# Kernel tuning notes

Measured on AMD Instinct MI355X. Metric: run time of the kernel, lower is better.

Reference implementation:

```python
import jax, jax.numpy as jnp
import numpy as np

NEG_INF = -9e15  # matches torch's -9000000000000000.0 mask value
ALPHA = 0.2      # leakyrelu slope for attention scores
OUT_SLOPE = 0.01 # default F.leaky_relu slope on the output


def setup_inputs() -> dict:
    key = jax.random.key(0)
    k = jax.random.split(key, 6)
    B, Ns, Nt = 4, 4096, 4096
    Fs, Ft, Fo = 256, 256, 64
    h = jax.random.normal(k[0], (B, Nt, Ft), dtype=jnp.float32)
    ctx = jax.random.normal(k[1], (B, Ns, Fs), dtype=jnp.float32)
    adj = jax.random.randint(k[2], (B, Nt, Ns), 0, 2, dtype=jnp.int32)
    Ws = jax.random.normal(k[3], (Fs, Fo), dtype=jnp.float32) * (1.414 * (6.0 / (Fs + Fo)) ** 0.5)
    Wt = jax.random.normal(k[4], (Ft, Fo), dtype=jnp.float32) * (1.414 * (6.0 / (Ft + Fo)) ** 0.5)
    a = jax.random.normal(k[5], (2 * Fo, 1), dtype=jnp.float32) * (1.414 * (6.0 / (2 * Fo + 1)) ** 0.5)
    return {"h": h, "ctx": ctx, "adj": adj, "Ws": Ws, "Wt": Wt, "a": a}


def _leaky(x, slope):
    return jnp.where(x > 0, x, slope * x)


def reference(h, ctx, adj, Ws, Wt, a):
    Fo = Ws.shape[1]
    Ws_ctx = jnp.einsum('bsf,fo->bso', ctx, Ws)   # [B, Ns, Fo]
    Wt_h = jnp.einsum('btf,fo->bto', h, Wt)       # [B, Nt, Fo]
    B, Ns, _ = Ws_ctx.shape
    Nt = Wt_h.shape[1]
    # a_input @ a decomposes: score(i,j) = Ws_ctx[i]@a[:Fo] + Wt_h[j]@a[Fo:]
    s = Ws_ctx @ a[:Fo, 0]  # [B, Ns]
    t = Wt_h @ a[Fo:, 0]    # [B, Nt]
    # Original builds flat order i*Nt + j (i over Ns, j over Nt), then views as [B, Nt, Ns].
    raw = s[:, :, None] + t[:, None, :]           # [B, Ns, Nt], flat index i*Nt+j
    e = _leaky(raw, ALPHA).reshape(B, Nt, Ns)     # faithful reshape
    masked = jnp.where(adj > 0, e, jnp.full_like(e, NEG_INF))
    attn = jax.nn.softmax(masked, axis=2)         # [B, Nt, Ns]
    h_prime = jnp.einsum('bts,bso->bto', attn, Ws_ctx)
    return _leaky(h_prime, OUT_SLOPE)
```

## Files before the change

### kernel.cpp

```cpp
#include <hip/hip_runtime.h>

#define BB 4
#define NS 4096
#define NT 4096
#define FS 256
#define FT 256
#define FO 64
#define ALPHA 0.2f
#define OUT_SLOPE 0.01f
#define L2E 1.4426950408889634f

typedef __attribute__((ext_vector_type(8))) short short8;
typedef __attribute__((ext_vector_type(4))) float floatx4;

__device__ __forceinline__ float leaky(float x, float s) { return x > 0.f ? x : s * x; }
__device__ __forceinline__ float leaky_max(float x, float s) { return fmaxf(x, s * x); }

__device__ __forceinline__ short f2bf(float x) {
  union { float f; unsigned u; } c; c.f = x;
  unsigned r = c.u + 0x7fffu + ((c.u >> 16) & 1u);
  return (short)(r >> 16);
}

__device__ __forceinline__ unsigned cvt_pk_bf16(float lo, float hi) {
  unsigned r;
  asm("v_cvt_pk_bf16_f32 %0, %1, %2" : "=v"(r) : "v"(lo), "v"(hi));
  return r;
}

__global__ void k_wa(const float* __restrict__ Wt, const float* __restrict__ a,
                     float* __restrict__ wa) {
  int f = threadIdx.x;
  float acc = 0.f;
#pragma unroll
  for (int o = 0; o < FO; ++o) acc += Wt[f * FO + o] * a[FO + o];
  wa[f] = acc * L2E;
}

__global__ __launch_bounds__(256) void k_t(const float* __restrict__ h,
                                           const float* __restrict__ wa,
                                           float* __restrict__ tvec) {
  int lane = threadIdx.x & 63, wave = threadIdx.x >> 6;
  int row = blockIdx.x * 4 + wave;
  const float4* hp = (const float4*)(h + (size_t)row * FT);
  const float4* wp = (const float4*)wa;
  float4 hv = hp[lane], wv = wp[lane];
  float acc = hv.x * wv.x + hv.y * wv.y + hv.z * wv.z + hv.w * wv.w;
#pragma unroll
  for (int off = 32; off; off >>= 1) acc += __shfl_down(acc, off);
  if (lane == 0) tvec[row] = acc;
}

__global__ __launch_bounds__(256) void k_tmax(const float* __restrict__ tvec,
                                              float* __restrict__ tmax) {
  __shared__ float red[256];
  int b = blockIdx.x, tid = threadIdx.x;
  float m = -3.0e38f;
  for (int j = tid; j < NS; j += 256) m = fmaxf(m, tvec[b * NS + j]);
  red[tid] = m;
  __syncthreads();
  for (int s = 128; s; s >>= 1) {
    if (tid < s) red[tid] = fmaxf(red[tid], red[tid + s]);
    __syncthreads();
  }
  if (tid == 0) tmax[b] = red[0];
}

__global__ __launch_bounds__(256) void k_wsctx(const float* __restrict__ ctx,
                                               const float* __restrict__ Ws,
                                               const float* __restrict__ a,
                                               short* __restrict__ vT,
                                               float* __restrict__ svec) {
  const int f = threadIdx.x & 63, wave = threadIdx.x >> 6;
  const int row0 = blockIdx.x * 16 + wave * 4;
  const float4* c0 = (const float4*)(ctx + (size_t)(row0 + 0) * FS);
  const float4* c1 = (const float4*)(ctx + (size_t)(row0 + 1) * FS);
  const float4* c2 = (const float4*)(ctx + (size_t)(row0 + 2) * FS);
  const float4* c3 = (const float4*)(ctx + (size_t)(row0 + 3) * FS);
  float r0 = 0.f, r1 = 0.f, r2 = 0.f, r3 = 0.f;
#pragma unroll 2
  for (int k4 = 0; k4 < FS / 4; ++k4) {
    const float w0 = Ws[(k4 * 4 + 0) * FO + f];
    const float w1 = Ws[(k4 * 4 + 1) * FO + f];
    const float w2 = Ws[(k4 * 4 + 2) * FO + f];
    const float w3 = Ws[(k4 * 4 + 3) * FO + f];
    float4 x;
    x = c0[k4]; r0 += x.x * w0 + x.y * w1 + x.z * w2 + x.w * w3;
    x = c1[k4]; r1 += x.x * w0 + x.y * w1 + x.z * w2 + x.w * w3;
    x = c2[k4]; r2 += x.x * w0 + x.y * w1 + x.z * w2 + x.w * w3;
    x = c3[k4]; r3 += x.x * w0 + x.y * w1 + x.z * w2 + x.w * w3;
  }
  const int b = row0 >> 12;
  const int rloc = row0 & (NS - 1);
  short* vp = vT + ((size_t)b * FO + f) * NS + rloc;
  vp[0] = f2bf(r0); vp[1] = f2bf(r1); vp[2] = f2bf(r2); vp[3] = f2bf(r3);

  const float af = a[f] * L2E;
  float s0 = r0 * af, s1 = r1 * af, s2 = r2 * af, s3 = r3 * af;
#pragma unroll
  for (int off = 32; off; off >>= 1) {
    s0 += __shfl_down(s0, off);
    s1 += __shfl_down(s1, off);
    s2 += __shfl_down(s2, off);
    s3 += __shfl_down(s3, off);
  }
  if (f == 0) {
    svec[row0 + 0] = s0;
    svec[row0 + 1] = s1;
    svec[row0 + 2] = s2;
    svec[row0 + 3] = s3;
  }
}

template <int JS>
__global__ __launch_bounds__(256) void k_part(const int* __restrict__ adj,
                                              const short* __restrict__ vT,
                                              const float* __restrict__ svec,
                                              const float* __restrict__ tvec,
                                              const float* __restrict__ tmax,
                                              float* __restrict__ outpart,
                                              float* __restrict__ lpart) {
  const int lane = threadIdx.x & 63;
  const int wv = threadIdx.x >> 6;
  const int m = lane & 15;
  const int q = lane >> 4;

  constexpr int LOG = (JS == 8) ? 3 : 2;
  const int tile = blockIdx.x >> LOG;
  const int js = blockIdx.x & (JS - 1);
  const int b = tile >> 6;
  const int i0 = (tile & 63) * 64;
  const int jbase = js * (NS / JS);

  const int r = i0 + wv * 16 + m;
  const float sr = svec[b * NS + r];
  const float cr = leaky_max(sr + tmax[b], ALPHA);

  const int* arow = adj + ((size_t)(b * NT) + r) * NS + jbase;
  const float* tp = tvec + b * NS + jbase;
  const short* vp0 = vT + ((size_t)b * FO + m) * NS + jbase;

  floatx4 acc0 = {0.f, 0.f, 0.f, 0.f};
  floatx4 acc1 = {0.f, 0.f, 0.f, 0.f};
  floatx4 acc2 = {0.f, 0.f, 0.f, 0.f};
  floatx4 acc3 = {0.f, 0.f, 0.f, 0.f};
  float lsum = 0.f;

#pragma unroll 2
  for (int jc = 0; jc < (NS / JS) / 32; ++jc) {
    const int j0 = jc * 32 + q * 8;
    const int4 a0 = *(const int4*)(arow + j0);
    const int4 a1 = *(const int4*)(arow + j0 + 4);
    const float4 t0 = *(const float4*)(tp + j0);
    const float4 t1 = *(const float4*)(tp + j0 + 4);

    float w[8];
    w[0] = (a0.x > 0) ? __builtin_amdgcn_exp2f(leaky_max(sr + t0.x, ALPHA) - cr) : 0.f;
    w[1] = (a0.y > 0) ? __builtin_amdgcn_exp2f(leaky_max(sr + t0.y, ALPHA) - cr) : 0.f;
    w[2] = (a0.z > 0) ? __builtin_amdgcn_exp2f(leaky_max(sr + t0.z, ALPHA) - cr) : 0.f;
    w[3] = (a0.w > 0) ? __builtin_amdgcn_exp2f(leaky_max(sr + t0.w, ALPHA) - cr) : 0.f;
    w[4] = (a1.x > 0) ? __builtin_amdgcn_exp2f(leaky_max(sr + t1.x, ALPHA) - cr) : 0.f;
    w[5] = (a1.y > 0) ? __builtin_amdgcn_exp2f(leaky_max(sr + t1.y, ALPHA) - cr) : 0.f;
    w[6] = (a1.z > 0) ? __builtin_amdgcn_exp2f(leaky_max(sr + t1.z, ALPHA) - cr) : 0.f;
    w[7] = (a1.w > 0) ? __builtin_amdgcn_exp2f(leaky_max(sr + t1.w, ALPHA) - cr) : 0.f;

    lsum += ((w[0] + w[1]) + (w[2] + w[3])) + ((w[4] + w[5]) + (w[6] + w[7]));

    union { short8 s; unsigned u[4]; } afu;
    afu.u[0] = cvt_pk_bf16(w[0], w[1]);
    afu.u[1] = cvt_pk_bf16(w[2], w[3]);
    afu.u[2] = cvt_pk_bf16(w[4], w[5]);
    afu.u[3] = cvt_pk_bf16(w[6], w[7]);
    const short8 af = afu.s;

    const short8 bf0 = *(const short8*)(vp0 + 0 * 16 * NS + j0);
    const short8 bf1 = *(const short8*)(vp0 + 1 * 16 * NS + j0);
    const short8 bf2 = *(const short8*)(vp0 + 2 * 16 * NS + j0);
    const short8 bf3 = *(const short8*)(vp0 + 3 * 16 * NS + j0);
    acc0 = __builtin_amdgcn_mfma_f32_16x16x32_bf16(af, bf0, acc0, 0, 0, 0);
    acc1 = __builtin_amdgcn_mfma_f32_16x16x32_bf16(af, bf1, acc1, 0, 0, 0);
    acc2 = __builtin_amdgcn_mfma_f32_16x16x32_bf16(af, bf2, acc2, 0, 0, 0);
    acc3 = __builtin_amdgcn_mfma_f32_16x16x32_bf16(af, bf3, acc3, 0, 0, 0);
  }

  float v = lsum;
  v += __shfl_down(v, 32);
  v += __shfl_down(v, 16);
  if (lane < 16) lpart[(size_t)js * BB * NT + (size_t)b * NT + i0 + wv * 16 + m] = v;

  float* op = outpart + (size_t)js * BB * NT * FO +
              ((size_t)(b * NT) + i0 + wv * 16 + q * 4) * FO + m;
#pragma unroll
  for (int reg = 0; reg < 4; ++reg) {
    op[(size_t)reg * FO + 0 * 16] = acc0[reg];
    op[(size_t)reg * FO + 1 * 16] = acc1[reg];
    op[(size_t)reg * FO + 2 * 16] = acc2[reg];
    op[(size_t)reg * FO + 3 * 16] = acc3[reg];
  }
}

template <int JS>
__global__ __launch_bounds__(256) void k_fin(const float* __restrict__ outpart,
                                             const float* __restrict__ lpart,
                                             float* __restrict__ out) {
  const size_t NP = (size_t)BB * NT * FO;
  const int idx = blockIdx.x * 256 + threadIdx.x;
  const int row = idx >> 4;
  float l = 0.f;
#pragma unroll
  for (int s = 0; s < JS; ++s) l += lpart[(size_t)s * BB * NT + row];
  const float inv = 1.f / l;
  float4 acc = {0.f, 0.f, 0.f, 0.f};
#pragma unroll
  for (int s = 0; s < JS; ++s) {
    float4 v = ((const float4*)(outpart + (size_t)s * NP))[idx];
    acc.x += v.x; acc.y += v.y; acc.z += v.z; acc.w += v.w;
  }
  float4 o;
  o.x = leaky_max(acc.x * inv, OUT_SLOPE);
  o.y = leaky_max(acc.y * inv, OUT_SLOPE);
  o.z = leaky_max(acc.z * inv, OUT_SLOPE);
  o.w = leaky_max(acc.w * inv, OUT_SLOPE);
  ((float4*)out)[idx] = o;
}

extern "C" void kernel_launch(void* const* d_in, const int* in_sizes, int n_in,
                              void* d_out, int out_size, void* d_ws, size_t ws_size,
                              hipStream_t stream) {
  const float* h   = (const float*)d_in[0];
  const float* ctx = (const float*)d_in[1];
  const int*   adj = (const int*)d_in[2];
  const float* Ws  = (const float*)d_in[3];
  const float* Wt  = (const float*)d_in[4];
  const float* a   = (const float*)d_in[5];
  float* out = (float*)d_out;
  float* ws = (float*)d_ws;

  const size_t np = (size_t)BB * NT * FO;
  const size_t fixed_f = 2 * (size_t)BB * NS + 256 + 4;
  const size_t vt_bytes = (size_t)BB * FO * NS * 2;
  const size_t need8 = ((size_t)8 * np + (size_t)8 * BB * NT + fixed_f) * sizeof(float) + vt_bytes;
  const int js = (ws_size >= need8) ? 8 : 4;

  float* outpart = ws;
  float* lpart   = outpart + (size_t)js * np;
  float* tvec    = lpart + (size_t)js * BB * NT;
  float* svec    = tvec + BB * NS;
  float* wa      = svec + BB * NS;
  float* tmax    = wa + 256;
  short* vT      = (short*)(tmax + 4);

  k_wa<<<1, 256, 0, stream>>>(Wt, a, wa);
  k_t<<<(BB * NT) / 4, 256, 0, stream>>>(h, wa, tvec);
  k_tmax<<<BB, 256, 0, stream>>>(tvec, tmax);
  k_wsctx<<<(BB * NS) / 16, 256, 0, stream>>>(ctx, Ws, a, vT, svec);
  if (js == 8) {
    k_part<8><<<(BB * NT / 64) * 8, 256, 0, stream>>>(adj, vT, svec, tvec, tmax,
                                                      outpart, lpart);
    k_fin<8><<<(BB * NT * FO / 4) / 256, 256, 0, stream>>>(outpart, lpart, out);
  } else {
    k_part<4><<<(BB * NT / 64) * 4, 256, 0, stream>>>(adj, vT, svec, tvec, tmax,
                                                      outpart, lpart);
    k_fin<4><<<(BB * NT * FO / 4) / 256, 256, 0, stream>>>(outpart, lpart, out);
  }
}
```

Measured before the change: 511.2 us.

## Software-pipeline k_part loads with double-buffered registers and fix split at 4

Restructures the main loop of the attention partial kernel into a two-stage register double buffer. The adj, t and V loads for the next chunk are issued before the exp/MFMA work on the current chunk, with scheduling barriers holding that order. It also adds a launch-bounds occupancy hint and hardcodes a j-split of 4 instead of picking 8 when workspace allows. The aim is to hide the latency of global loads from the streamed adjacency; the costs are higher register pressure and, if 8 was being chosen before, fewer blocks in flight.

```diff
diff --git a/kernel.cpp b/kernel.cpp
--- a/kernel.cpp
+++ b/kernel.cpp
@@ -8,12 +8,12 @@
 #define FO 64
 #define ALPHA 0.2f
 #define OUT_SLOPE 0.01f
+#define JSPLIT 4
 #define L2E 1.4426950408889634f
 
 typedef __attribute__((ext_vector_type(8))) short short8;
 typedef __attribute__((ext_vector_type(4))) float floatx4;
 
-__device__ __forceinline__ float leaky(float x, float s) { return x > 0.f ? x : s * x; }
 __device__ __forceinline__ float leaky_max(float x, float s) { return fmaxf(x, s * x); }
 
 __device__ __forceinline__ short f2bf(float x) {
@@ -113,19 +113,20 @@
 }
 
 template <int JS>
-__global__ __launch_bounds__(256) void k_part(const int* __restrict__ adj,
-                                              const short* __restrict__ vT,
-                                              const float* __restrict__ svec,
-                                              const float* __restrict__ tvec,
-                                              const float* __restrict__ tmax,
-                                              float* __restrict__ outpart,
-                                              float* __restrict__ lpart) {
+__global__ __launch_bounds__(256, 4) void k_part(const int* __restrict__ adj,
+                                                 const short* __restrict__ vT,
+                                                 const float* __restrict__ svec,
+                                                 const float* __restrict__ tvec,
+                                                 const float* __restrict__ tmax,
+                                                 float* __restrict__ outpart,
+                                                 float* __restrict__ lpart) {
   const int lane = threadIdx.x & 63;
   const int wv = threadIdx.x >> 6;
   const int m = lane & 15;
   const int q = lane >> 4;
 
   constexpr int LOG = (JS == 8) ? 3 : 2;
+  constexpr int NC = (NS / JS) / 32;
   const int tile = blockIdx.x >> LOG;
   const int js = blockIdx.x & (JS - 1);
   const int b = tile >> 6;
@@ -146,42 +147,60 @@
   floatx4 acc3 = {0.f, 0.f, 0.f, 0.f};
   float lsum = 0.f;
 
-#pragma unroll 2
-  for (int jc = 0; jc < (NS / JS) / 32; ++jc) {
-    const int j0 = jc * 32 + q * 8;
-    const int4 a0 = *(const int4*)(arow + j0);
-    const int4 a1 = *(const int4*)(arow + j0 + 4);
-    const float4 t0 = *(const float4*)(tp + j0);
-    const float4 t1 = *(const float4*)(tp + j0 + 4);
-
-    float w[8];
-    w[0] = (a0.x > 0) ? __builtin_amdgcn_exp2f(leaky_max(sr + t0.x, ALPHA) - cr) : 0.f;
-    w[1] = (a0.y > 0) ? __builtin_amdgcn_exp2f(leaky_max(sr + t0.y, ALPHA) - cr) : 0.f;
-    w[2] = (a0.z > 0) ? __builtin_amdgcn_exp2f(leaky_max(sr + t0.z, ALPHA) - cr) : 0.f;
-    w[3] = (a0.w > 0) ? __builtin_amdgcn_exp2f(leaky_max(sr + t0.w, ALPHA) - cr) : 0.f;
-    w[4] = (a1.x > 0) ? __builtin_amdgcn_exp2f(leaky_max(sr + t1.x, ALPHA) - cr) : 0.f;
-    w[5] = (a1.y > 0) ? __builtin_amdgcn_exp2f(leaky_max(sr + t1.y, ALPHA) - cr) : 0.f;
-    w[6] = (a1.z > 0) ? __builtin_amdgcn_exp2f(leaky_max(sr + t1.z, ALPHA) - cr) : 0.f;
-    w[7] = (a1.w > 0) ? __builtin_amdgcn_exp2f(leaky_max(sr + t1.w, ALPHA) - cr) : 0.f;
-
-    lsum += ((w[0] + w[1]) + (w[2] + w[3])) + ((w[4] + w[5]) + (w[6] + w[7]));
-
-    union { short8 s; unsigned u[4]; } afu;
-    afu.u[0] = cvt_pk_bf16(w[0], w[1]);
-    afu.u[1] = cvt_pk_bf16(w[2], w[3]);
-    afu.u[2] = cvt_pk_bf16(w[4], w[5]);
-    afu.u[3] = cvt_pk_bf16(w[6], w[7]);
-    const short8 af = afu.s;
-
-    const short8 bf0 = *(const short8*)(vp0 + 0 * 16 * NS + j0);
-    const short8 bf1 = *(const short8*)(vp0 + 1 * 16 * NS + j0);
-    const short8 bf2 = *(const short8*)(vp0 + 2 * 16 * NS + j0);
-    const short8 bf3 = *(const short8*)(vp0 + 3 * 16 * NS + j0);
-    acc0 = __builtin_amdgcn_mfma_f32_16x16x32_bf16(af, bf0, acc0, 0, 0, 0);
-    acc1 = __builtin_amdgcn_mfma_f32_16x16x32_bf16(af, bf1, acc1, 0, 0, 0);
-    acc2 = __builtin_amdgcn_mfma_f32_16x16x32_bf16(af, bf2, acc2, 0, 0, 0);
-    acc3 = __builtin_amdgcn_mfma_f32_16x16x32_bf16(af, bf3, acc3, 0, 0, 0);
-  }
+  int4 Aa0, Aa1; float4 At0, At1; short8 Av0, Av1, Av2, Av3;
+  int4 Ba0, Ba1; float4 Bt0, Bt1; short8 Bv0, Bv1, Bv2, Bv3;
+
+#define ISSUE(S, jc) do {                                        \
+    const int j0_ = (jc) * 32 + q * 8;                           \
+    S##a0 = *(const int4*)(arow + j0_);                          \
+    S##a1 = *(const int4*)(arow + j0_ + 4);                      \
+    S##t0 = *(const float4*)(tp + j0_);                          \
+    S##t1 = *(const float4*)(tp + j0_ + 4);                      \
+    S##v0 = *(const short8*)(vp0 + 0 * 16 * NS + j0_);           \
+    S##v1 = *(const short8*)(vp0 + 1 * 16 * NS + j0_);           \
+    S##v2 = *(const short8*)(vp0 + 2 * 16 * NS + j0_);           \
+    S##v3 = *(const short8*)(vp0 + 3 * 16 * NS + j0_);           \
+  } while (0)
+
+#define COMPUTE(S) do {                                                         \
+    float w0 = (S##a0.x > 0) ? __builtin_amdgcn_exp2f(leaky_max(sr + S##t0.x, ALPHA) - cr) : 0.f; \
+    float w1 = (S##a0.y > 0) ? __builtin_amdgcn_exp2f(leaky_max(sr + S##t0.y, ALPHA) - cr) : 0.f; \
+    float w2 = (S##a0.z > 0) ? __builtin_amdgcn_exp2f(leaky_max(sr + S##t0.z, ALPHA) - cr) : 0.f; \
+    float w3 = (S##a0.w > 0) ? __builtin_amdgcn_exp2f(leaky_max(sr + S##t0.w, ALPHA) - cr) : 0.f; \
+    float w4 = (S##a1.x > 0) ? __builtin_amdgcn_exp2f(leaky_max(sr + S##t1.x, ALPHA) - cr) : 0.f; \
+    float w5 = (S##a1.y > 0) ? __builtin_amdgcn_exp2f(leaky_max(sr + S##t1.y, ALPHA) - cr) : 0.f; \
+    float w6 = (S##a1.z > 0) ? __builtin_amdgcn_exp2f(leaky_max(sr + S##t1.z, ALPHA) - cr) : 0.f; \
+    float w7 = (S##a1.w > 0) ? __builtin_amdgcn_exp2f(leaky_max(sr + S##t1.w, ALPHA) - cr) : 0.f; \
+    lsum += ((w0 + w1) + (w2 + w3)) + ((w4 + w5) + (w6 + w7));                 \
+    union { short8 s; unsigned u[4]; } afu_;                                    \
+    afu_.u[0] = cvt_pk_bf16(w0, w1);                                            \
+    afu_.u[1] = cvt_pk_bf16(w2, w3);                                            \
+    afu_.u[2] = cvt_pk_bf16(w4, w5);                                            \
+    afu_.u[3] = cvt_pk_bf16(w6, w7);                                            \
+    const short8 af_ = afu_.s;                                                  \
+    acc0 = __builtin_amdgcn_mfma_f32_16x16x32_bf16(af_, S##v0, acc0, 0, 0, 0);  \
+    acc1 = __builtin_amdgcn_mfma_f32_16x16x32_bf16(af_, S##v1, acc1, 0, 0, 0);  \
+    acc2 = __builtin_amdgcn_mfma_f32_16x16x32_bf16(af_, S##v2, acc2, 0, 0, 0);  \
+    acc3 = __builtin_amdgcn_mfma_f32_16x16x32_bf16(af_, S##v3, acc3, 0, 0, 0);  \
+  } while (0)
+
+  ISSUE(A, 0);
+  __builtin_amdgcn_sched_barrier(0);
+#pragma unroll 1
+  for (int c = 0; c < NC - 2; c += 2) {
+    ISSUE(B, c + 1);
+    __builtin_amdgcn_sched_barrier(0);
+    COMPUTE(A);
+    ISSUE(A, c + 2);
+    __builtin_amdgcn_sched_barrier(0);
+    COMPUTE(B);
+  }
+  ISSUE(B, NC - 1);
+  __builtin_amdgcn_sched_barrier(0);
+  COMPUTE(A);
+  COMPUTE(B);
+#undef ISSUE
+#undef COMPUTE
 
   float v = lsum;
   v += __shfl_down(v, 32);
@@ -236,15 +255,9 @@
   float* out = (float*)d_out;
   float* ws = (float*)d_ws;
 
-  const size_t np = (size_t)BB * NT * FO;
-  const size_t fixed_f = 2 * (size_t)BB * NS + 256 + 4;
-  const size_t vt_bytes = (size_t)BB * FO * NS * 2;
-  const size_t need8 = ((size_t)8 * np + (size_t)8 * BB * NT + fixed_f) * sizeof(float) + vt_bytes;
-  const int js = (ws_size >= need8) ? 8 : 4;
-
   float* outpart = ws;
-  float* lpart   = outpart + (size_t)js * np;
-  float* tvec    = lpart + (size_t)js * BB * NT;
+  float* lpart   = outpart + (size_t)JSPLIT * BB * NT * FO;
+  float* tvec    = lpart + (size_t)JSPLIT * BB * NT;
   float* svec    = tvec + BB * NS;
   float* wa      = svec + BB * NS;
   float* tmax    = wa + 256;
@@ -254,13 +267,7 @@
   k_t<<<(BB * NT) / 4, 256, 0, stream>>>(h, wa, tvec);
   k_tmax<<<BB, 256, 0, stream>>>(tvec, tmax);
   k_wsctx<<<(BB * NS) / 16, 256, 0, stream>>>(ctx, Ws, a, vT, svec);
-  if (js == 8) {
-    k_part<8><<<(BB * NT / 64) * 8, 256, 0, stream>>>(adj, vT, svec, tvec, tmax,
-                                                      outpart, lpart);
-    k_fin<8><<<(BB * NT * FO / 4) / 256, 256, 0, stream>>>(outpart, lpart, out);
-  } else {
-    k_part<4><<<(BB * NT / 64) * 4, 256, 0, stream>>>(adj, vT, svec, tvec, tmax,
-                                                      outpart, lpart);
-    k_fin<4><<<(BB * NT * FO / 4) / 256, 256, 0, stream>>>(outpart, lpart, out);
-  }
-}
+  k_part<JSPLIT><<<(BB * NT / 64) * JSPLIT, 256, 0, stream>>>(adj, vT, svec, tvec,
+                                                              tmax, outpart, lpart);
+  k_fin<JSPLIT><<<(BB * NT * FO / 4) / 256, 256, 0, stream>>>(outpart, lpart, out);
+}
```

Result: faster. 492.4 us, median of 2 (-3.7%).
